# Performance work log

Hardware: AMD Instinct MI355X
Metric: run time of the kernel (lower is better)

## Reference

```python
import jax, jax.numpy as jnp
import numpy as np

B, SQ, SK, DK, DV = 8, 2048, 2048, 256, 256
EPS = 1e-7  # keras.backend.epsilon()


def setup_inputs() -> dict:
    key = jax.random.key(0)
    kq, kk, kv, km = jax.random.split(key, 4)
    query = jax.random.normal(kq, (B, SQ, DK), dtype=jnp.float32)
    k_ = jax.random.normal(kk, (B, SK, DK), dtype=jnp.float32)
    value = jax.random.normal(kv, (B, SK, DV), dtype=jnp.float32)
    mask = jax.random.uniform(km, (B, SK)) > 0.1
    return {"query": query, "key": k_, "value": value, "mask": mask}


def reference(query, key, value, mask):
    d = query.shape[-1]
    # scores: [B, Sq, Sk]
    e = jnp.einsum('bqd,bkd->bqk', query, key) / jnp.sqrt(jnp.asarray(d, query.dtype))
    # original applies exp(e - max) BEFORE masking (non-standard but faithful)
    e = jnp.exp(e - jnp.max(e, axis=-1, keepdims=True))
    q_len, k_len = query.shape[1], key.shape[1]
    causal = (jnp.arange(k_len)[None, :] <= jnp.arange(q_len)[:, None]).astype(query.dtype)
    e = e * causal[None, :, :]                       # history_only mask
    e = e * mask[:, None, :].astype(query.dtype)     # key padding mask
    a = e / (jnp.sum(e, axis=-1, keepdims=True) + EPS)
    return jnp.einsum('bqk,bkv->bqv', a, value)
```

## Files before the change

kernel.cpp:

```cpp
#include <hip/hip_runtime.h>
#include <hip/hip_bf16.h>

#define B_   8
#define SQ_  2048
#define SK_  2048
#define DK_  256
#define DV_  256

#define KT    32
#define PSTR  40
#define TELEM (KT * DK_)
#define NQB   16

typedef __bf16 bf16x8 __attribute__((ext_vector_type(8)));
typedef float  f32x4  __attribute__((ext_vector_type(4)));

__device__ __forceinline__ void gl_lds16(const void* g, void* l) {
    __builtin_amdgcn_global_load_lds(
        (const __attribute__((address_space(1))) void*)g,
        (__attribute__((address_space(3))) void*)l, 16, 0, 0);
}

__global__ __launch_bounds__(256)
void make_tiles(const float* __restrict__ K, const float* __restrict__ V,
                __bf16* __restrict__ Kt, __bf16* __restrict__ Vt)
{
    const int t = blockIdx.x, b = blockIdx.y;
    {
        __bf16* out = Kt + ((size_t)(b * 64 + t)) * TELEM;
        const float* src = K + ((size_t)(b * SK_ + t * KT)) * DK_;
        #pragma unroll
        for (int it = 0; it < 4; ++it) {
            int ci  = it * 256 + threadIdx.x;
            int dk8 = ci >> 5;
            int key = ci & 31;
            const float* p = src + (size_t)key * DK_ + dk8 * 8;
            float4 f0 = *(const float4*)(p);
            float4 f1 = *(const float4*)(p + 4);
            bf16x8 o;
            o[0] = (__bf16)f0.x; o[1] = (__bf16)f0.y; o[2] = (__bf16)f0.z; o[3] = (__bf16)f0.w;
            o[4] = (__bf16)f1.x; o[5] = (__bf16)f1.y; o[6] = (__bf16)f1.z; o[7] = (__bf16)f1.w;
            *(bf16x8*)(out + (size_t)ci * 8) = o;
        }
    }
    {
        __bf16* out = Vt + ((size_t)(b * 64 + t)) * TELEM;
        const float* src = V + ((size_t)(b * SK_ + t * KT)) * DV_;
        #pragma unroll
        for (int it = 0; it < 4; ++it) {
            int ci  = it * 256 + threadIdx.x;
            int kc8 = ci >> 8;
            int dv  = ci & 255;
            const float* p = src + (size_t)(kc8 * 8) * DV_ + dv;
            bf16x8 o;
            #pragma unroll
            for (int j = 0; j < 8; ++j)
                o[j] = (__bf16)p[(size_t)j * DV_];
            *(bf16x8*)(out + (size_t)ci * 8) = o;
        }
    }
}

__global__ __launch_bounds__(512, 4)
void attn_fwd(const float* __restrict__ Qg, const __bf16* __restrict__ Kt,
              const __bf16* __restrict__ Vt, const void* __restrict__ Mv,
              __bf16* __restrict__ Opart, float* __restrict__ Lpart,
              int tpc, int slotcap)
{
    __shared__ __align__(16) __bf16 sK[2][TELEM];
    __shared__ __align__(16) __bf16 sV[2][TELEM];
    __shared__ __align__(16) __bf16 sP[8][16 * PSTR];

    const int tid  = threadIdx.x;
    const int wv   = tid >> 6;
    const int lane = tid & 63;
    const int quad = lane >> 4;
    const int l16  = lane & 15;

    const int b = blockIdx.x;

    int yy = blockIdx.y, qb = 0, s = 0;
    for (int q = NQB - 1; q >= 0; --q) {
        int c = (4 * (q + 1) + tpc - 1) / tpc;
        if (yy < c) { qb = q; s = yy; break; }
        yy -= c;
    }
    const int nt = 4 * (qb + 1);
    const int nc = (nt + tpc - 1) / tpc;
    const int t0 = nt * s / nc;
    const int t1 = nt * (s + 1) / nc;

    const int qrow = qb * 128 + wv * 16;

    const unsigned char* Mb = (const unsigned char*)Mv;
    const int*           Mi = (const int*)Mv;
    int nzb = 0;
    {
        const unsigned int* mw = (const unsigned int*)Mv;
        #pragma unroll
        for (int i = 0; i < 32; ++i) {
            unsigned int w = mw[i];
            nzb += ((w & 0x000000ffu) != 0) + ((w & 0x0000ff00u) != 0)
                 + ((w & 0x00ff0000u) != 0) + ((w & 0xff000000u) != 0);
        }
    }
    const bool mask_byte = (nzb > 40);

    bf16x8 qfrag[8];
    {
        const float* qp = Qg + ((size_t)(b * SQ_ + qrow + l16)) * DK_ + quad * 8;
        #pragma unroll
        for (int kt = 0; kt < 8; ++kt) {
            float4 f0 = *(const float4*)(qp + kt * 32);
            float4 f1 = *(const float4*)(qp + kt * 32 + 4);
            bf16x8 q;
            q[0] = (__bf16)f0.x; q[1] = (__bf16)f0.y; q[2] = (__bf16)f0.z; q[3] = (__bf16)f0.w;
            q[4] = (__bf16)f1.x; q[5] = (__bf16)f1.y; q[6] = (__bf16)f1.z; q[7] = (__bf16)f1.w;
            qfrag[kt] = q;
        }
    }

    f32x4 oacc[16];
    #pragma unroll
    for (int v = 0; v < 16; ++v) oacc[v] = (f32x4){0.f, 0.f, 0.f, 0.f};
    float lsum[4] = {0.f, 0.f, 0.f, 0.f};

    const __bf16* Kbase = Kt + (size_t)b * 64 * TELEM;
    const __bf16* Vbase = Vt + (size_t)b * 64 * TELEM;
    const size_t  mbase = (size_t)b * SK_;

    {
        const __bf16* kg = Kbase + (size_t)t0 * TELEM;
        const __bf16* vg = Vbase + (size_t)t0 * TELEM;
        #pragma unroll
        for (int r = 0; r < 2; ++r) {
            int ci = r * 512 + tid;
            gl_lds16(kg + (size_t)ci * 8, (char*)&sK[0][0] + ci * 16);
            gl_lds16(vg + (size_t)ci * 8, (char*)&sV[0][0] + ci * 16);
        }
    }
    __syncthreads();

    int cur = 0;
    for (int t = t0; t < t1; ++t) {
        if (t + 1 < t1) {
            const __bf16* kg = Kbase + (size_t)(t + 1) * TELEM;
            const __bf16* vg = Vbase + (size_t)(t + 1) * TELEM;
            #pragma unroll
            for (int r = 0; r < 2; ++r) {
                int ci = r * 512 + tid;
                gl_lds16(kg + (size_t)ci * 8, (char*)&sK[cur ^ 1][0] + ci * 16);
                gl_lds16(vg + (size_t)ci * 8, (char*)&sV[cur ^ 1][0] + ci * 16);
            }
        }

        const int k0 = t * KT;

        f32x4 s0 = {0.f,0.f,0.f,0.f}, s1 = {0.f,0.f,0.f,0.f};
        #pragma unroll
        for (int kt = 0; kt < 8; ++kt) {
            bf16x8 b0 = *(const bf16x8*)&sK[cur][(size_t)((kt * 4 + quad) * 32 + l16)      * 8];
            bf16x8 b1 = *(const bf16x8*)&sK[cur][(size_t)((kt * 4 + quad) * 32 + 16 + l16) * 8];
            s0 = __builtin_amdgcn_mfma_f32_16x16x32_bf16(qfrag[kt], b0, s0, 0, 0, 0);
            s1 = __builtin_amdgcn_mfma_f32_16x16x32_bf16(qfrag[kt], b1, s1, 0, 0, 0);
        }

        #pragma unroll
        for (int nf = 0; nf < 2; ++nf) {
            f32x4 sv = (nf == 0) ? s0 : s1;
            int key = k0 + nf * 16 + l16;
            float mk = mask_byte ? (Mb[mbase + key] ? 1.0f : 0.0f)
                                 : (Mi[mbase + key] ? 1.0f : 0.0f);
            #pragma unroll
            for (int i = 0; i < 4; ++i) {
                int qr = qrow + quad * 4 + i;
                float p = __expf(sv[i] * 0.0625f);
                p = (key <= qr) ? (p * mk) : 0.0f;
                lsum[i] += p;
                sP[wv][(quad * 4 + i) * PSTR + nf * 16 + l16] = (__bf16)p;
            }
        }
        asm volatile("s_waitcnt lgkmcnt(0)" ::: "memory");
        __builtin_amdgcn_wave_barrier();

        {
            bf16x8 pa = *(const bf16x8*)&sP[wv][l16 * PSTR + quad * 8];
            #pragma unroll
            for (int vf = 0; vf < 16; ++vf) {
                bf16x8 bv = *(const bf16x8*)&sV[cur][(size_t)(quad * 256 + vf * 16 + l16) * 8];
                oacc[vf] = __builtin_amdgcn_mfma_f32_16x16x32_bf16(pa, bv, oacc[vf], 0, 0, 0);
            }
        }

        __syncthreads();
        cur ^= 1;
    }

    const size_t slot = ((size_t)(b * NQB + qb)) * slotcap + s;
    #pragma unroll
    for (int i = 0; i < 4; ++i) {
        float v = lsum[i];
        v += __shfl_xor(v, 1);
        v += __shfl_xor(v, 2);
        v += __shfl_xor(v, 4);
        v += __shfl_xor(v, 8);
        lsum[i] = v;
    }
    if (l16 == 0) {
        #pragma unroll
        for (int i = 0; i < 4; ++i)
            Lpart[slot * 128 + wv * 16 + quad * 4 + i] = lsum[i];
    }
    __bf16* ob = Opart + slot * (size_t)(128 * 256);
    #pragma unroll
    for (int vf = 0; vf < 16; ++vf) {
        #pragma unroll
        for (int i = 0; i < 4; ++i)
            ob[(wv * 16 + quad * 4 + i) * 256 + vf * 16 + l16] = (__bf16)oacc[vf][i];
    }
}

__global__ __launch_bounds__(512)
void attn_reduce(const __bf16* __restrict__ Opart, const float* __restrict__ Lpart,
                 float* __restrict__ Og, int tpc, int slotcap)
{
    const int b    = blockIdx.x;
    const int y    = blockIdx.y;
    const int qb64 = y >> 1;
    const int half = y & 1;
    const int qb   = qb64 >> 1;
    const int rowbase = (qb64 & 1) * 64;
    const int nt   = 4 * (qb + 1);
    const int chunks = (nt + tpc - 1) / tpc;
    const int tid  = threadIdx.x;
    const int row  = tid >> 3;
    const int cg   = tid & 7;

    const size_t sbase = ((size_t)(b * NQB + qb)) * slotcap;
    float acc[16];
    #pragma unroll
    for (int i = 0; i < 16; ++i) acc[i] = 0.f;
    float ls = 0.f;

    for (int s = 0; s < chunks; ++s) {
        const __bf16* p = Opart + (sbase + s) * (size_t)(128 * 256)
                        + (size_t)(rowbase + row) * 256 + half * 128 + cg * 16;
        bf16x8 x0 = *(const bf16x8*)(p);
        bf16x8 x1 = *(const bf16x8*)(p + 8);
        #pragma unroll
        for (int e = 0; e < 8; ++e) { acc[e] += (float)x0[e]; acc[8 + e] += (float)x1[e]; }
        ls += Lpart[(sbase + s) * 128 + rowbase + row];
    }
    const float inv = 1.0f / (ls + 1e-7f);
    float* op = Og + ((size_t)b * SQ_ + qb64 * 64 + row) * DV_ + half * 128 + cg * 16;
    #pragma unroll
    for (int v = 0; v < 4; ++v) {
        float4 o;
        o.x = acc[v * 4 + 0] * inv; o.y = acc[v * 4 + 1] * inv;
        o.z = acc[v * 4 + 2] * inv; o.w = acc[v * 4 + 3] * inv;
        *(float4*)(op + v * 4) = o;
    }
}

extern "C" void kernel_launch(void* const* d_in, const int* in_sizes, int n_in,
                              void* d_out, int out_size, void* d_ws, size_t ws_size,
                              hipStream_t stream) {
    const float* Q = (const float*)d_in[0];
    const float* K = (const float*)d_in[1];
    const float* V = (const float*)d_in[2];
    const void*  M = d_in[3];
    float* Out = (float*)d_out;

    __bf16* Ktl = (__bf16*)d_ws;
    __bf16* Vtl = Ktl + (size_t)B_ * 64 * TELEM;
    __bf16* Opart = Vtl + (size_t)B_ * 64 * TELEM;

    auto need = [](int slotcap) -> size_t {
        return (size_t)(16 * 1024 * 1024)
             + (size_t)(B_ * NQB) * slotcap * (128 * 256) * 2
             + (size_t)(B_ * NQB) * slotcap * 128 * 4;
    };
    int tpc, slotcap;
    if      (ws_size >= need(8)) { tpc = 8;  slotcap = 8; }
    else if (ws_size >= need(4)) { tpc = 16; slotcap = 4; }
    else                         { tpc = 64; slotcap = 1; }
    int nch = 0;
    for (int q = 0; q < NQB; ++q) nch += (4 * (q + 1) + tpc - 1) / tpc;

    float* Lpart = (float*)(Opart + (size_t)(B_ * NQB) * slotcap * (128 * 256));

    make_tiles<<<dim3(64, B_), dim3(256), 0, stream>>>(K, V, Ktl, Vtl);
    attn_fwd<<<dim3(B_, nch), dim3(512), 0, stream>>>(Q, Ktl, Vtl, M, Opart, Lpart,
                                                      tpc, slotcap);
    attn_reduce<<<dim3(B_, 64), dim3(512), 0, stream>>>(Opart, Lpart, Out, tpc, slotcap);
}
```

Measured before the change: 152.5 us.

## Fuse split-K reduction into attention kernel via last-block atomic counter

Removes the separate reduce kernel. Each attention block now bumps a per-(batch, query block) atomic counter, and the last block to finish sums the partial outputs and denominators and writes the final result. The V tiling pass is rewritten to use float4 loads, counters are zeroed inside make_tiles, and tiles per chunk change from 8 to 10. This saves a launch and lets the reduction overlap with other blocks, at the cost of serialized tail work in the last block and extra fences.

Result: slower. 330.9 us (+116.9%).

```diff
diff --git a/kernel.cpp b/kernel.cpp
--- a/kernel.cpp
+++ b/kernel.cpp
@@ -23,9 +23,12 @@
 
 __global__ __launch_bounds__(256)
 void make_tiles(const float* __restrict__ K, const float* __restrict__ V,
-                __bf16* __restrict__ Kt, __bf16* __restrict__ Vt)
+                __bf16* __restrict__ Kt, __bf16* __restrict__ Vt,
+                int* __restrict__ cnt)
 {
-    const int t = blockIdx.x, b = blockIdx.y;
+    const int b = blockIdx.x, t = blockIdx.y;
+    if (b == 0 && t == 0 && threadIdx.x < B_ * NQB)
+        cnt[threadIdx.x] = 0;
     {
         __bf16* out = Kt + ((size_t)(b * 64 + t)) * TELEM;
         const float* src = K + ((size_t)(b * SK_ + t * KT)) * DK_;
@@ -46,18 +49,21 @@
     {
         __bf16* out = Vt + ((size_t)(b * 64 + t)) * TELEM;
         const float* src = V + ((size_t)(b * SK_ + t * KT)) * DV_;
-        #pragma unroll
-        for (int it = 0; it < 4; ++it) {
-            int ci  = it * 256 + threadIdx.x;
-            int kc8 = ci >> 8;
-            int dv  = ci & 255;
-            const float* p = src + (size_t)(kc8 * 8) * DV_ + dv;
-            bf16x8 o;
-            #pragma unroll
-            for (int j = 0; j < 8; ++j)
-                o[j] = (__bf16)p[(size_t)j * DV_];
-            *(bf16x8*)(out + (size_t)ci * 8) = o;
-        }
+        int kc8 = threadIdx.x >> 6;
+        int dv4 = threadIdx.x & 63;
+        const float* p = src + (size_t)(kc8 * 8) * DV_ + dv4 * 4;
+        bf16x8 o0, o1, o2, o3;
+        #pragma unroll
+        for (int j = 0; j < 8; ++j) {
+            float4 f = *(const float4*)(p + (size_t)j * DV_);
+            o0[j] = (__bf16)f.x; o1[j] = (__bf16)f.y;
+            o2[j] = (__bf16)f.z; o3[j] = (__bf16)f.w;
+        }
+        __bf16* q = out + (size_t)(kc8 * 256 + dv4 * 4) * 8;
+        *(bf16x8*)(q)      = o0;
+        *(bf16x8*)(q + 8)  = o1;
+        *(bf16x8*)(q + 16) = o2;
+        *(bf16x8*)(q + 24) = o3;
     }
 }
 
@@ -65,11 +71,13 @@
 void attn_fwd(const float* __restrict__ Qg, const __bf16* __restrict__ Kt,
               const __bf16* __restrict__ Vt, const void* __restrict__ Mv,
               __bf16* __restrict__ Opart, float* __restrict__ Lpart,
+              float* __restrict__ Og, int* __restrict__ cnt,
               int tpc, int slotcap)
 {
     __shared__ __align__(16) __bf16 sK[2][TELEM];
     __shared__ __align__(16) __bf16 sV[2][TELEM];
     __shared__ __align__(16) __bf16 sP[8][16 * PSTR];
+    __shared__ int s_old;
 
     const int tid  = threadIdx.x;
     const int wv   = tid >> 6;
@@ -218,47 +226,44 @@
         for (int i = 0; i < 4; ++i)
             ob[(wv * 16 + quad * 4 + i) * 256 + vf * 16 + l16] = (__bf16)oacc[vf][i];
     }
-}
-
-__global__ __launch_bounds__(512)
-void attn_reduce(const __bf16* __restrict__ Opart, const float* __restrict__ Lpart,
-                 float* __restrict__ Og, int tpc, int slotcap)
-{
-    const int b    = blockIdx.x;
-    const int y    = blockIdx.y;
-    const int qb64 = y >> 1;
-    const int half = y & 1;
-    const int qb   = qb64 >> 1;
-    const int rowbase = (qb64 & 1) * 64;
-    const int nt   = 4 * (qb + 1);
-    const int chunks = (nt + tpc - 1) / tpc;
-    const int tid  = threadIdx.x;
-    const int row  = tid >> 3;
-    const int cg   = tid & 7;
-
-    const size_t sbase = ((size_t)(b * NQB + qb)) * slotcap;
-    float acc[16];
+
+    __threadfence();
+    __syncthreads();
+    if (tid == 0) s_old = atomicAdd(&cnt[b * NQB + qb], 1);
+    __syncthreads();
+    if (s_old != nc - 1) return;
+    __threadfence();
+
+    const size_t sb2 = ((size_t)(b * NQB + qb)) * slotcap;
+    const int row = tid >> 2;
+    const int cg  = tid & 3;
+    float ls = 0.f;
+    for (int sdx = 0; sdx < nc; ++sdx)
+        ls += Lpart[(sb2 + sdx) * 128 + row];
+    const float inv = 1.0f / (ls + 1e-7f);
     #pragma unroll
-    for (int i = 0; i < 16; ++i) acc[i] = 0.f;
-    float ls = 0.f;
-
-    for (int s = 0; s < chunks; ++s) {
-        const __bf16* p = Opart + (sbase + s) * (size_t)(128 * 256)
-                        + (size_t)(rowbase + row) * 256 + half * 128 + cg * 16;
-        bf16x8 x0 = *(const bf16x8*)(p);
-        bf16x8 x1 = *(const bf16x8*)(p + 8);
-        #pragma unroll
-        for (int e = 0; e < 8; ++e) { acc[e] += (float)x0[e]; acc[8 + e] += (float)x1[e]; }
-        ls += Lpart[(sbase + s) * 128 + rowbase + row];
-    }
-    const float inv = 1.0f / (ls + 1e-7f);
-    float* op = Og + ((size_t)b * SQ_ + qb64 * 64 + row) * DV_ + half * 128 + cg * 16;
-    #pragma unroll
-    for (int v = 0; v < 4; ++v) {
-        float4 o;
-        o.x = acc[v * 4 + 0] * inv; o.y = acc[v * 4 + 1] * inv;
-        o.z = acc[v * 4 + 2] * inv; o.w = acc[v * 4 + 3] * inv;
-        *(float4*)(op + v * 4) = o;
+    for (int h = 0; h < 2; ++h) {
+        float acc[32];
+        #pragma unroll
+        for (int i = 0; i < 32; ++i) acc[i] = 0.f;
+        for (int sdx = 0; sdx < nc; ++sdx) {
+            const __bf16* p = Opart + (sb2 + sdx) * (size_t)(128 * 256)
+                            + (size_t)row * 256 + cg * 64 + h * 32;
+            #pragma unroll
+            for (int v = 0; v < 4; ++v) {
+                bf16x8 x = *(const bf16x8*)(p + v * 8);
+                #pragma unroll
+                for (int e = 0; e < 8; ++e) acc[v * 8 + e] += (float)x[e];
+            }
+        }
+        float* op = Og + ((size_t)b * SQ_ + qb * 128 + row) * DV_ + cg * 64 + h * 32;
+        #pragma unroll
+        for (int v = 0; v < 8; ++v) {
+            float4 o;
+            o.x = acc[v * 4 + 0] * inv; o.y = acc[v * 4 + 1] * inv;
+            o.z = acc[v * 4 + 2] * inv; o.w = acc[v * 4 + 3] * inv;
+            *(float4*)(op + v * 4) = o;
+        }
     }
 }
 
@@ -278,19 +283,20 @@
     auto need = [](int slotcap) -> size_t {
         return (size_t)(16 * 1024 * 1024)
              + (size_t)(B_ * NQB) * slotcap * (128 * 256) * 2
-             + (size_t)(B_ * NQB) * slotcap * 128 * 4;
+             + (size_t)(B_ * NQB) * slotcap * 128 * 4
+             + 512;
     };
     int tpc, slotcap;
-    if      (ws_size >= need(8)) { tpc = 8;  slotcap = 8; }
+    if      (ws_size >= need(8)) { tpc = 10; slotcap = 8; }
     else if (ws_size >= need(4)) { tpc = 16; slotcap = 4; }
     else                         { tpc = 64; slotcap = 1; }
     int nch = 0;
     for (int q = 0; q < NQB; ++q) nch += (4 * (q + 1) + tpc - 1) / tpc;
 
     float* Lpart = (float*)(Opart + (size_t)(B_ * NQB) * slotcap * (128 * 256));
-
-    make_tiles<<<dim3(64, B_), dim3(256), 0, stream>>>(K, V, Ktl, Vtl);
+    int*   cnt   = (int*)(Lpart + (size_t)(B_ * NQB) * slotcap * 128);
+
+    make_tiles<<<dim3(B_, 64), dim3(256), 0, stream>>>(K, V, Ktl, Vtl, cnt);
     attn_fwd<<<dim3(B_, nch), dim3(512), 0, stream>>>(Q, Ktl, Vtl, M, Opart, Lpart,
-                                                      tpc, slotcap);
-    attn_reduce<<<dim3(B_, 64), dim3(512), 0, stream>>>(Opart, Lpart, Out, tpc, slotcap);
+                                                      Out, cnt, tpc, slotcap);
 }
```

## Give each wave 32 query rows to reuse K/V LDS fragments

Applied to the files above, without the earlier changes.

The attention kernel moves from 8 waves × 16 query rows to 4 waves × 32 query rows per block. Each K and V fragment read from LDS now feeds two MFMAs, halving LDS traffic per unit of matrix work. The cost is more accumulator and Q-fragment registers per wave, and launch bounds drop to 256 threads with a minimum of 2 blocks. The tiles-per-chunk split changes from 8 to 10, and the V transpose in make_tiles now uses float4 loads, with its grid axes swapped.

New measurement: 139.8 us. 1.09x faster.

```diff
diff --git a/kernel.cpp b/kernel.cpp
--- a/kernel.cpp
+++ b/kernel.cpp
@@ -25,7 +25,7 @@
 void make_tiles(const float* __restrict__ K, const float* __restrict__ V,
                 __bf16* __restrict__ Kt, __bf16* __restrict__ Vt)
 {
-    const int t = blockIdx.x, b = blockIdx.y;
+    const int b = blockIdx.x, t = blockIdx.y;
     {
         __bf16* out = Kt + ((size_t)(b * 64 + t)) * TELEM;
         const float* src = K + ((size_t)(b * SK_ + t * KT)) * DK_;
@@ -46,22 +46,25 @@
     {
         __bf16* out = Vt + ((size_t)(b * 64 + t)) * TELEM;
         const float* src = V + ((size_t)(b * SK_ + t * KT)) * DV_;
-        #pragma unroll
-        for (int it = 0; it < 4; ++it) {
-            int ci  = it * 256 + threadIdx.x;
-            int kc8 = ci >> 8;
-            int dv  = ci & 255;
-            const float* p = src + (size_t)(kc8 * 8) * DV_ + dv;
-            bf16x8 o;
-            #pragma unroll
-            for (int j = 0; j < 8; ++j)
-                o[j] = (__bf16)p[(size_t)j * DV_];
-            *(bf16x8*)(out + (size_t)ci * 8) = o;
-        }
-    }
-}
-
-__global__ __launch_bounds__(512, 4)
+        int kc8 = threadIdx.x >> 6;
+        int dv4 = threadIdx.x & 63;
+        const float* p = src + (size_t)(kc8 * 8) * DV_ + dv4 * 4;
+        bf16x8 o0, o1, o2, o3;
+        #pragma unroll
+        for (int j = 0; j < 8; ++j) {
+            float4 f = *(const float4*)(p + (size_t)j * DV_);
+            o0[j] = (__bf16)f.x; o1[j] = (__bf16)f.y;
+            o2[j] = (__bf16)f.z; o3[j] = (__bf16)f.w;
+        }
+        __bf16* q = out + (size_t)(kc8 * 256 + dv4 * 4) * 8;
+        *(bf16x8*)(q)      = o0;
+        *(bf16x8*)(q + 8)  = o1;
+        *(bf16x8*)(q + 16) = o2;
+        *(bf16x8*)(q + 24) = o3;
+    }
+}
+
+__global__ __launch_bounds__(256, 2)
 void attn_fwd(const float* __restrict__ Qg, const __bf16* __restrict__ Kt,
               const __bf16* __restrict__ Vt, const void* __restrict__ Mv,
               __bf16* __restrict__ Opart, float* __restrict__ Lpart,
@@ -69,7 +72,7 @@
 {
     __shared__ __align__(16) __bf16 sK[2][TELEM];
     __shared__ __align__(16) __bf16 sV[2][TELEM];
-    __shared__ __align__(16) __bf16 sP[8][16 * PSTR];
+    __shared__ __align__(16) __bf16 sP[4][32 * PSTR];
 
     const int tid  = threadIdx.x;
     const int wv   = tid >> 6;
@@ -90,7 +93,7 @@
     const int t0 = nt * s / nc;
     const int t1 = nt * (s + 1) / nc;
 
-    const int qrow = qb * 128 + wv * 16;
+    const int qrow = qb * 128 + wv * 32;
 
     const unsigned char* Mb = (const unsigned char*)Mv;
     const int*           Mi = (const int*)Mv;
@@ -106,9 +109,10 @@
     }
     const bool mask_byte = (nzb > 40);
 
-    bf16x8 qfrag[8];
-    {
-        const float* qp = Qg + ((size_t)(b * SQ_ + qrow + l16)) * DK_ + quad * 8;
+    bf16x8 qfrag[2][8];
+    #pragma unroll
+    for (int rs = 0; rs < 2; ++rs) {
+        const float* qp = Qg + ((size_t)(b * SQ_ + qrow + rs * 16 + l16)) * DK_ + quad * 8;
         #pragma unroll
         for (int kt = 0; kt < 8; ++kt) {
             float4 f0 = *(const float4*)(qp + kt * 32);
@@ -116,14 +120,16 @@
             bf16x8 q;
             q[0] = (__bf16)f0.x; q[1] = (__bf16)f0.y; q[2] = (__bf16)f0.z; q[3] = (__bf16)f0.w;
             q[4] = (__bf16)f1.x; q[5] = (__bf16)f1.y; q[6] = (__bf16)f1.z; q[7] = (__bf16)f1.w;
-            qfrag[kt] = q;
-        }
-    }
-
-    f32x4 oacc[16];
-    #pragma unroll
-    for (int v = 0; v < 16; ++v) oacc[v] = (f32x4){0.f, 0.f, 0.f, 0.f};
-    float lsum[4] = {0.f, 0.f, 0.f, 0.f};
+            qfrag[rs][kt] = q;
+        }
+    }
+
+    f32x4 oacc[2][16];
+    #pragma unroll
+    for (int rs = 0; rs < 2; ++rs)
+        #pragma unroll
+        for (int v = 0; v < 16; ++v) oacc[rs][v] = (f32x4){0.f, 0.f, 0.f, 0.f};
+    float lsum[2][4] = {{0.f,0.f,0.f,0.f},{0.f,0.f,0.f,0.f}};
 
     const __bf16* Kbase = Kt + (size_t)b * 64 * TELEM;
     const __bf16* Vbase = Vt + (size_t)b * 64 * TELEM;
@@ -133,8 +139,8 @@
         const __bf16* kg = Kbase + (size_t)t0 * TELEM;
         const __bf16* vg = Vbase + (size_t)t0 * TELEM;
         #pragma unroll
-        for (int r = 0; r < 2; ++r) {
-            int ci = r * 512 + tid;
+        for (int r = 0; r < 4; ++r) {
+            int ci = r * 256 + tid;
             gl_lds16(kg + (size_t)ci * 8, (char*)&sK[0][0] + ci * 16);
             gl_lds16(vg + (size_t)ci * 8, (char*)&sV[0][0] + ci * 16);
         }
@@ -147,8 +153,8 @@
             const __bf16* kg = Kbase + (size_t)(t + 1) * TELEM;
             const __bf16* vg = Vbase + (size_t)(t + 1) * TELEM;
             #pragma unroll
-            for (int r = 0; r < 2; ++r) {
-                int ci = r * 512 + tid;
+            for (int r = 0; r < 4; ++r) {
+                int ci = r * 256 + tid;
                 gl_lds16(kg + (size_t)ci * 8, (char*)&sK[cur ^ 1][0] + ci * 16);
                 gl_lds16(vg + (size_t)ci * 8, (char*)&sV[cur ^ 1][0] + ci * 16);
             }
@@ -156,39 +162,48 @@
 
         const int k0 = t * KT;
 
-        f32x4 s0 = {0.f,0.f,0.f,0.f}, s1 = {0.f,0.f,0.f,0.f};
+        f32x4 s00 = {0.f,0.f,0.f,0.f}, s01 = {0.f,0.f,0.f,0.f};
+        f32x4 s10 = {0.f,0.f,0.f,0.f}, s11 = {0.f,0.f,0.f,0.f};
         #pragma unroll
         for (int kt = 0; kt < 8; ++kt) {
             bf16x8 b0 = *(const bf16x8*)&sK[cur][(size_t)((kt * 4 + quad) * 32 + l16)      * 8];
             bf16x8 b1 = *(const bf16x8*)&sK[cur][(size_t)((kt * 4 + quad) * 32 + 16 + l16) * 8];
-            s0 = __builtin_amdgcn_mfma_f32_16x16x32_bf16(qfrag[kt], b0, s0, 0, 0, 0);
-            s1 = __builtin_amdgcn_mfma_f32_16x16x32_bf16(qfrag[kt], b1, s1, 0, 0, 0);
+            s00 = __builtin_amdgcn_mfma_f32_16x16x32_bf16(qfrag[0][kt], b0, s00, 0, 0, 0);
+            s01 = __builtin_amdgcn_mfma_f32_16x16x32_bf16(qfrag[0][kt], b1, s01, 0, 0, 0);
+            s10 = __builtin_amdgcn_mfma_f32_16x16x32_bf16(qfrag[1][kt], b0, s10, 0, 0, 0);
+            s11 = __builtin_amdgcn_mfma_f32_16x16x32_bf16(qfrag[1][kt], b1, s11, 0, 0, 0);
         }
 
         #pragma unroll
         for (int nf = 0; nf < 2; ++nf) {
-            f32x4 sv = (nf == 0) ? s0 : s1;
             int key = k0 + nf * 16 + l16;
             float mk = mask_byte ? (Mb[mbase + key] ? 1.0f : 0.0f)
                                  : (Mi[mbase + key] ? 1.0f : 0.0f);
             #pragma unroll
-            for (int i = 0; i < 4; ++i) {
-                int qr = qrow + quad * 4 + i;
-                float p = __expf(sv[i] * 0.0625f);
-                p = (key <= qr) ? (p * mk) : 0.0f;
-                lsum[i] += p;
-                sP[wv][(quad * 4 + i) * PSTR + nf * 16 + l16] = (__bf16)p;
+            for (int rs = 0; rs < 2; ++rs) {
+                f32x4 sv = (rs == 0) ? ((nf == 0) ? s00 : s01)
+                                     : ((nf == 0) ? s10 : s11);
+                #pragma unroll
+                for (int i = 0; i < 4; ++i) {
+                    int qr = qrow + rs * 16 + quad * 4 + i;
+                    float p = __expf(sv[i] * 0.0625f);
+                    p = (key <= qr) ? (p * mk) : 0.0f;
+                    lsum[rs][i] += p;
+                    sP[wv][(rs * 16 + quad * 4 + i) * PSTR + nf * 16 + l16] = (__bf16)p;
+                }
             }
         }
         asm volatile("s_waitcnt lgkmcnt(0)" ::: "memory");
         __builtin_amdgcn_wave_barrier();
 
         {
-            bf16x8 pa = *(const bf16x8*)&sP[wv][l16 * PSTR + quad * 8];
+            bf16x8 pa0 = *(const bf16x8*)&sP[wv][(l16)      * PSTR + quad * 8];
+            bf16x8 pa1 = *(const bf16x8*)&sP[wv][(16 + l16) * PSTR + quad * 8];
             #pragma unroll
             for (int vf = 0; vf < 16; ++vf) {
                 bf16x8 bv = *(const bf16x8*)&sV[cur][(size_t)(quad * 256 + vf * 16 + l16) * 8];
-                oacc[vf] = __builtin_amdgcn_mfma_f32_16x16x32_bf16(pa, bv, oacc[vf], 0, 0, 0);
+                oacc[0][vf] = __builtin_amdgcn_mfma_f32_16x16x32_bf16(pa0, bv, oacc[0][vf], 0, 0, 0);
+                oacc[1][vf] = __builtin_amdgcn_mfma_f32_16x16x32_bf16(pa1, bv, oacc[1][vf], 0, 0, 0);
             }
         }
 
@@ -198,26 +213,32 @@
 
     const size_t slot = ((size_t)(b * NQB + qb)) * slotcap + s;
     #pragma unroll
-    for (int i = 0; i < 4; ++i) {
-        float v = lsum[i];
-        v += __shfl_xor(v, 1);
-        v += __shfl_xor(v, 2);
-        v += __shfl_xor(v, 4);
-        v += __shfl_xor(v, 8);
-        lsum[i] = v;
-    }
+    for (int rs = 0; rs < 2; ++rs)
+        #pragma unroll
+        for (int i = 0; i < 4; ++i) {
+            float v = lsum[rs][i];
+            v += __shfl_xor(v, 1);
+            v += __shfl_xor(v, 2);
+            v += __shfl_xor(v, 4);
+            v += __shfl_xor(v, 8);
+            lsum[rs][i] = v;
+        }
     if (l16 == 0) {
         #pragma unroll
-        for (int i = 0; i < 4; ++i)
-            Lpart[slot * 128 + wv * 16 + quad * 4 + i] = lsum[i];
+        for (int rs = 0; rs < 2; ++rs)
+            #pragma unroll
+            for (int i = 0; i < 4; ++i)
+                Lpart[slot * 128 + wv * 32 + rs * 16 + quad * 4 + i] = lsum[rs][i];
     }
     __bf16* ob = Opart + slot * (size_t)(128 * 256);
     #pragma unroll
-    for (int vf = 0; vf < 16; ++vf) {
-        #pragma unroll
-        for (int i = 0; i < 4; ++i)
-            ob[(wv * 16 + quad * 4 + i) * 256 + vf * 16 + l16] = (__bf16)oacc[vf][i];
-    }
+    for (int rs = 0; rs < 2; ++rs)
+        #pragma unroll
+        for (int vf = 0; vf < 16; ++vf)
+            #pragma unroll
+            for (int i = 0; i < 4; ++i)
+                ob[(wv * 32 + rs * 16 + quad * 4 + i) * 256 + vf * 16 + l16]
+                    = (__bf16)oacc[rs][vf][i];
 }
 
 __global__ __launch_bounds__(512)
@@ -281,7 +302,7 @@
              + (size_t)(B_ * NQB) * slotcap * 128 * 4;
     };
     int tpc, slotcap;
-    if      (ws_size >= need(8)) { tpc = 8;  slotcap = 8; }
+    if      (ws_size >= need(8)) { tpc = 10; slotcap = 8; }
     else if (ws_size >= need(4)) { tpc = 16; slotcap = 4; }
     else                         { tpc = 64; slotcap = 1; }
     int nch = 0;
@@ -289,8 +310,8 @@
 
     float* Lpart = (float*)(Opart + (size_t)(B_ * NQB) * slotcap * (128 * 256));
 
-    make_tiles<<<dim3(64, B_), dim3(256), 0, stream>>>(K, V, Ktl, Vtl);
-    attn_fwd<<<dim3(B_, nch), dim3(512), 0, stream>>>(Q, Ktl, Vtl, M, Opart, Lpart,
+    make_tiles<<<dim3(B_, 64), dim3(256), 0, stream>>>(K, V, Ktl, Vtl);
+    attn_fwd<<<dim3(B_, nch), dim3(256), 0, stream>>>(Q, Ktl, Vtl, M, Opart, Lpart,
                                                       tpc, slotcap);
     attn_reduce<<<dim3(B_, 64), dim3(512), 0, stream>>>(Opart, Lpart, Out, tpc, slotcap);
 }
```
